# Optimization experiments

Hardware: AMD Instinct MI355X
Metric: run time of the kernel (lower is better)

The kernel has to match this reference:

```python
import jax, jax.numpy as jnp
import numpy as np

B, S, E, H = 4, 4096, 1024, 16
W_SIZE, LB, LF = 128, 1, 1   # window size, look_backward, look_forward (non-causal)
HD = E // H                  # head dim = 64
NW = S // W_SIZE             # num windows = 32
NC = LB + LF + 1             # concatenated windows per query window = 3


def collect_windows(x, backward=LB, forward=LF, pad_value=-1):
    # x: [BH, NW, w] or [BH, NW, w, d]; gather windows i-backward..i+forward
    nw = x.shape[1]
    pad = [(0, 0), (backward, forward)] + [(0, 0)] * (x.ndim - 2)
    xp = jnp.pad(x, pad, constant_values=pad_value)  # faithful: pads k/v with -1 like the torch code
    g = jnp.stack([xp[:, j:j + nw] for j in range(backward + forward + 1)], axis=2)  # [BH,NW,NC,w,...]
    if x.ndim == 4:
        return g.reshape(x.shape[0], nw, NC * x.shape[2], x.shape[3])
    return g.reshape(x.shape[0], nw, NC * x.shape[2])


def setup_inputs() -> dict:
    key = jax.random.key(0)
    k1, k2 = jax.random.split(key)
    x = jax.random.normal(k1, (B, S, E), dtype=jnp.float32)
    w_qkv = jax.random.normal(k2, (E, 3 * E), dtype=jnp.float32) * 0.02
    b_qkv = jnp.zeros((3 * E,), dtype=jnp.float32)
    return {"x": x, "w_qkv": w_qkv, "b_qkv": b_qkv}


def reference(x, w_qkv, b_qkv):
    qkv = x @ w_qkv + b_qkv                                   # [B,S,3E]
    q, k, v = jnp.split(qkv, 3, axis=-1)

    def to_heads(t):
        return t.reshape(B, S, H, HD).transpose(0, 2, 1, 3).reshape(B * H, S, HD)

    q, k, v = to_heads(q), to_heads(k), to_heads(v)

    bq = q.reshape(B * H, NW, W_SIZE, HD)                     # [BH,NW,w,d]
    bk = collect_windows(k.reshape(B * H, NW, W_SIZE, HD))    # [BH,NW,NC*w,d]
    bv = collect_windows(v.reshape(B * H, NW, W_SIZE, HD))

    t = jnp.arange(S, dtype=jnp.int32).reshape(1, NW, W_SIZE)
    ct = collect_windows(t)                                   # [1,NW,NC*w], pads are -1

    # no 1/sqrt(d) scaling in the original module
    scores = jnp.einsum('bnqd,bnkd->bnqk', bq, bk)            # [BH,NW,w,NC*w]

    qi = t.reshape(1, NW, W_SIZE, 1)                          # query absolute positions
    ctb = ct[:, :, None, :]                                   # key absolute positions
    max_i = qi + W_SIZE * LF
    min_i = qi - W_SIZE * LB
    overcompute = ((ctb > max_i) | (ctb < min_i)) & (ctb != -1)

    scores = jnp.where(overcompute, -jnp.inf, scores)
    attn = jax.nn.softmax(scores, axis=-1)
    attn = jnp.nan_to_num(attn, nan=0.0, posinf=0.0, neginf=0.0)

    out = jnp.einsum('bnqk,bnkd->bnqd', attn, bv)             # [BH,NW,w,d]
    out = out.reshape(B, H, S, HD).transpose(0, 2, 1, 3).reshape(B, S, E)
    return out
```

## Files before the change

### kernel.cpp

```cpp
#include <hip/hip_runtime.h>
#include <hip/hip_bf16.h>
#include <cmath>

constexpr int Bn  = 4;
constexpr int Sn  = 4096;
constexpr int En  = 1024;
constexpr int Hn  = 16;
constexpr int HD  = 64;
constexpr int WSZ = 128;
constexpr int NW  = Sn / WSZ;
constexpr int Mr  = Bn * Sn;
constexpr int N3  = 3 * En;
constexpr int Kd  = En;

typedef __attribute__((ext_vector_type(8))) short  bf16x8;
typedef __attribute__((ext_vector_type(4))) float  f32x4;
typedef __attribute__((ext_vector_type(8))) unsigned short ushort8;

__device__ __forceinline__ unsigned short f2bf(float f) {
  __hip_bfloat16 h = __float2bfloat16(f);
  return *reinterpret_cast<unsigned short*>(&h);
}

__device__ __forceinline__ void gload_lds16(const void* g, void* l) {
  __builtin_amdgcn_global_load_lds(
      (const __attribute__((address_space(1))) void*)g,
      (__attribute__((address_space(3))) void*)l, 16, 0, 0);
}

__global__ __launch_bounds__(256) void cvt_x(const float* __restrict__ x,
                                             unsigned short* __restrict__ xb) {
  const int i = (blockIdx.x * 256 + threadIdx.x) * 8;
  const float4 a = *(const float4*)&x[i];
  const float4 b = *(const float4*)&x[i + 4];
  ushort8 o;
  o[0] = f2bf(a.x); o[1] = f2bf(a.y); o[2] = f2bf(a.z); o[3] = f2bf(a.w);
  o[4] = f2bf(b.x); o[5] = f2bf(b.y); o[6] = f2bf(b.z); o[7] = f2bf(b.w);
  *(ushort8*)&xb[i] = o;
}

__global__ __launch_bounds__(256) void cvt_wT(const float* __restrict__ W,
                                              unsigned short* __restrict__ Wt) {
  __shared__ float t[32][33];
  const int bx = blockIdx.x * 32;
  const int by = blockIdx.y * 32;
  const int tx = threadIdx.x & 31;
  const int ty = threadIdx.x >> 5;
  #pragma unroll
  for (int i = 0; i < 32; i += 8)
    t[ty + i][tx] = W[(size_t)(by + ty + i) * N3 + bx + tx];
  __syncthreads();
  #pragma unroll
  for (int i = 0; i < 32; i += 8)
    Wt[(size_t)(bx + ty + i) * Kd + by + tx] = f2bf(t[tx][ty + i]);
}

constexpr int TM = 128, TN = 128, TK = 32;

__global__ __launch_bounds__(256) void qkv_gemm_bf16(
    const unsigned short* __restrict__ Abf,
    const unsigned short* __restrict__ Bt,
    const float* __restrict__ bias,
    unsigned short* __restrict__ Qb, unsigned short* __restrict__ Kb,
    unsigned short* __restrict__ Vb) {
  __shared__ unsigned short As[TM * TK];
  __shared__ unsigned short Bs[TN * TK];

  const int tid  = threadIdx.x;
  const int wave = tid >> 6;
  const int lane = tid & 63;
  const int bm = blockIdx.y * TM;
  const int bn = blockIdx.x * TN;
  const int wr = wave >> 1, wc = wave & 1;

  f32x4 acc[4][4] = {};

  const int sr  = lane >> 2;
  const int sc8 = (lane & 3) * 8;
  const int fr = lane & 15;
  const int fk = (lane >> 4) * 8;

  for (int k0 = 0; k0 < Kd; k0 += TK) {
    #pragma unroll
    for (int i = 0; i < 2; ++i) {
      const int c = wave * 2 + i;
      gload_lds16(Abf + (size_t)(bm + c * 16 + sr) * Kd + k0 + sc8, &As[c * 512]);
      gload_lds16(Bt  + (size_t)(bn + c * 16 + sr) * Kd + k0 + sc8, &Bs[c * 512]);
    }
    __syncthreads();
    bf16x8 af[4], bfr[4];
    #pragma unroll
    for (int m = 0; m < 4; ++m)
      af[m] = *(const bf16x8*)&As[(wr * 64 + m * 16 + fr) * TK + fk];
    #pragma unroll
    for (int n = 0; n < 4; ++n)
      bfr[n] = *(const bf16x8*)&Bs[(wc * 64 + n * 16 + fr) * TK + fk];
    #pragma unroll
    for (int m = 0; m < 4; ++m)
      #pragma unroll
      for (int n = 0; n < 4; ++n)
        acc[m][n] = __builtin_amdgcn_mfma_f32_16x16x32_bf16(
            af[m], bfr[n], acc[m][n], 0, 0, 0);
    __syncthreads();
  }

  const int col0 = bn + wc * 64 + (lane & 15);
  const int row0 = bm + wr * 64 + (lane >> 4) * 4;
  #pragma unroll
  for (int n = 0; n < 4; ++n) {
    const int col = col0 + n * 16;
    const float bv = bias[col];
    const int which = col >> 10;
    const int h = (col >> 6) & 15;
    const int d = col & 63;
    unsigned short* T = (which == 0) ? Qb : (which == 1) ? Kb : Vb;
    #pragma unroll
    for (int m = 0; m < 4; ++m)
      #pragma unroll
      for (int r = 0; r < 4; ++r) {
        const int row = row0 + m * 16 + r;
        const int b = row >> 12;
        const int s = row & 4095;
        T[((size_t)((b << 4) + h) * Sn + s) * HD + d] =
            f2bf(acc[m][n][r] + bv);
      }
  }
}

__global__ __launch_bounds__(256) void attn_mfma(
    const unsigned short* __restrict__ Qb,
    const unsigned short* __restrict__ Kb,
    const unsigned short* __restrict__ Vb,
    float* __restrict__ out) {
  __shared__ unsigned short Qs[128 * 64];
  __shared__ unsigned short Ks[64 * 64];
  __shared__ unsigned short Vt[64 * 64];
  __shared__ unsigned short Ps[4][32 * 72];

  const int w   = blockIdx.x;
  const int bh  = blockIdx.y;
  const int tid = threadIdx.x, wave = tid >> 6, lane = tid & 63;
  const int gl = lane >> 4;
  const int li = lane & 15;
  const int q0 = wave * 32;

  const size_t head_off = (size_t)bh * Sn * HD;
  const unsigned short* Qg = Qb + head_off + (size_t)w * WSZ * HD;

  const int rsub = lane >> 3;
  const int bsub = ((lane & 7) ^ rsub) << 3;
  #pragma unroll
  for (int i = 0; i < 4; ++i) {
    const int c = wave * 4 + i;
    gload_lds16(Qg + (size_t)(c * 8 + rsub) * HD + bsub, &Qs[c * 512]);
  }
  __syncthreads();

  auto lds_frag = [&](const unsigned short* base, int row, int kpos) {
    return *(const bf16x8*)((const char*)base + row * 128 +
                            ((kpos * 2) ^ ((row & 7) << 4)));
  };

  bf16x8 ones;
  #pragma unroll
  for (int j = 0; j < 8; ++j) ones[j] = (short)0x3F80;
  f32x4 qsum[2] = {};
  #pragma unroll
  for (int m = 0; m < 2; ++m)
    #pragma unroll
    for (int ks = 0; ks < 2; ++ks)
      qsum[m] = __builtin_amdgcn_mfma_f32_16x16x32_bf16(
          lds_frag(Qs, q0 + m * 16 + li, ks * 32 + gl * 8), ones, qsum[m], 0, 0, 0);

  f32x4 acc[2][4] = {};
  float m_run[2][4], l_run[2][4];
  #pragma unroll
  for (int m = 0; m < 2; ++m)
    #pragma unroll
    for (int r = 0; r < 4; ++r) { m_run[m][r] = -3e38f; l_run[m][r] = 0.f; }

  unsigned short* Psw = &Ps[wave][0];
  const int vkey = wave * 16 + (lane >> 2);
  const int vd0 = (lane & 3) * 16;

  for (int c = 0; c < 3; ++c) {
    const int wk = w + c - 1;
    if (wk < 0 || wk >= NW) {
      #pragma unroll
      for (int m = 0; m < 2; ++m)
        #pragma unroll
        for (int r = 0; r < 4; ++r) {
          const float sp = -qsum[m][r];
          const float mn = fmaxf(m_run[m][r], sp);
          const float scale = __expf(m_run[m][r] - mn);
          const float pe = __expf(sp - mn) * 128.f;
          l_run[m][r] = l_run[m][r] * scale + pe;
          m_run[m][r] = mn;
          #pragma unroll
          for (int nd = 0; nd < 4; ++nd)
            acc[m][nd][r] = acc[m][nd][r] * scale - pe;
        }
      continue;
    }
    for (int ch = 0; ch < 2; ++ch) {
      __syncthreads();
      const unsigned short* Kg =
          Kb + head_off + (size_t)(wk * WSZ + ch * 64) * HD;
      #pragma unroll
      for (int i = 0; i < 2; ++i) {
        const int cc = wave * 2 + i;
        gload_lds16(Kg + (size_t)(cc * 8 + rsub) * HD + bsub, &Ks[cc * 512]);
      }
      {
        const unsigned short* Vg =
            Vb + head_off + (size_t)(wk * WSZ + ch * 64) * HD;
        const ushort8 v0 = *(const ushort8*)&Vg[vkey * HD + vd0];
        const ushort8 v1 = *(const ushort8*)&Vg[vkey * HD + vd0 + 8];
        #pragma unroll
        for (int j = 0; j < 8; ++j) {
          int d = vd0 + j;
          *(unsigned short*)((char*)Vt + ((d * 128 + vkey * 2) ^ ((d & 7) << 4))) = v0[j];
          d = vd0 + 8 + j;
          *(unsigned short*)((char*)Vt + ((d * 128 + vkey * 2) ^ ((d & 7) << 4))) = v1[j];
        }
      }
      __syncthreads();

      f32x4 s[2][4] = {};
      #pragma unroll
      for (int ks = 0; ks < 2; ++ks) {
        const bf16x8 aq0 = lds_frag(Qs, q0 + li, ks * 32 + gl * 8);
        const bf16x8 aq1 = lds_frag(Qs, q0 + 16 + li, ks * 32 + gl * 8);
        #pragma unroll
        for (int n = 0; n < 4; ++n) {
          const bf16x8 bk = lds_frag(Ks, n * 16 + li, ks * 32 + gl * 8);
          s[0][n] = __builtin_amdgcn_mfma_f32_16x16x32_bf16(aq0, bk, s[0][n], 0, 0, 0);
          s[1][n] = __builtin_amdgcn_mfma_f32_16x16x32_bf16(aq1, bk, s[1][n], 0, 0, 0);
        }
      }
      if (c != 1) {
        #pragma unroll
        for (int m = 0; m < 2; ++m)
          #pragma unroll
          for (int n = 0; n < 4; ++n)
            #pragma unroll
            for (int r = 0; r < 4; ++r) {
              const int q_in = q0 + m * 16 + gl * 4 + r;
              const int k_in = ch * 64 + n * 16 + li;
              const bool bad = (c == 0) ? (k_in < q_in) : (k_in > q_in);
              if (bad) s[m][n][r] = -3e38f;
            }
      }
      #pragma unroll
      for (int m = 0; m < 2; ++m) {
        float mx[4], sc[4], rs[4];
        #pragma unroll
        for (int r = 0; r < 4; ++r)
          mx[r] = fmaxf(fmaxf(s[m][0][r], s[m][1][r]),
                        fmaxf(s[m][2][r], s[m][3][r]));
        #pragma unroll
        for (int off = 1; off < 16; off <<= 1)
          #pragma unroll
          for (int r = 0; r < 4; ++r)
            mx[r] = fmaxf(mx[r], __shfl_xor(mx[r], off));
        #pragma unroll
        for (int r = 0; r < 4; ++r) {
          const float mn = fmaxf(m_run[m][r], mx[r]);
          sc[r] = __expf(m_run[m][r] - mn);
          m_run[m][r] = mn;
          rs[r] = 0.f;
        }
        #pragma unroll
        for (int n = 0; n < 4; ++n)
          #pragma unroll
          for (int r = 0; r < 4; ++r) {
            const float v = s[m][n][r];
            const float p = (v > -1e30f) ? __expf(v - m_run[m][r]) : 0.f;
            s[m][n][r] = p;
            rs[r] += p;
          }
        #pragma unroll
        for (int off = 1; off < 16; off <<= 1)
          #pragma unroll
          for (int r = 0; r < 4; ++r)
            rs[r] += __shfl_xor(rs[r], off);
        #pragma unroll
        for (int r = 0; r < 4; ++r)
          l_run[m][r] = l_run[m][r] * sc[r] + rs[r];
        #pragma unroll
        for (int nd = 0; nd < 4; ++nd)
          #pragma unroll
          for (int r = 0; r < 4; ++r)
            acc[m][nd][r] *= sc[r];
      }
      #pragma unroll
      for (int m = 0; m < 2; ++m)
        #pragma unroll
        for (int n = 0; n < 4; ++n)
          #pragma unroll
          for (int r = 0; r < 4; ++r)
            Psw[(m * 16 + gl * 4 + r) * 72 + n * 16 + li] = f2bf(s[m][n][r]);
      #pragma unroll
      for (int ks = 0; ks < 2; ++ks) {
        const bf16x8 ap0 = *(const bf16x8*)&Psw[(li) * 72 + ks * 32 + gl * 8];
        const bf16x8 ap1 = *(const bf16x8*)&Psw[(16 + li) * 72 + ks * 32 + gl * 8];
        #pragma unroll
        for (int nd = 0; nd < 4; ++nd) {
          const bf16x8 bv = lds_frag(Vt, nd * 16 + li, ks * 32 + gl * 8);
          acc[0][nd] = __builtin_amdgcn_mfma_f32_16x16x32_bf16(ap0, bv, acc[0][nd], 0, 0, 0);
          acc[1][nd] = __builtin_amdgcn_mfma_f32_16x16x32_bf16(ap1, bv, acc[1][nd], 0, 0, 0);
        }
      }
    }
  }

  const int b = bh >> 4, h = bh & 15;
  #pragma unroll
  for (int m = 0; m < 2; ++m) {
    float inv[4];
    #pragma unroll
    for (int r = 0; r < 4; ++r) inv[r] = 1.f / l_run[m][r];
    #pragma unroll
    for (int nd = 0; nd < 4; ++nd)
      #pragma unroll
      for (int r = 0; r < 4; ++r) {
        const int q = q0 + m * 16 + gl * 4 + r;
        out[((size_t)(b * Sn + w * WSZ + q)) * En + h * HD + nd * 16 + li] =
            acc[m][nd][r] * inv[r];
      }
  }
}

extern "C" void kernel_launch(void* const* d_in, const int* in_sizes, int n_in,
                              void* d_out, int out_size, void* d_ws,
                              size_t ws_size, hipStream_t stream) {
  const float* x    = (const float*)d_in[0];
  const float* wqkv = (const float*)d_in[1];
  const float* bqkv = (const float*)d_in[2];
  float* out = (float*)d_out;

  unsigned short* ws = (unsigned short*)d_ws;
  const size_t HT = (size_t)Bn * Hn * Sn * HD;
  unsigned short* Qb = ws;
  unsigned short* Kb = ws + HT;
  unsigned short* Vb = ws + 2 * HT;
  unsigned short* xb = ws + 3 * HT;
  unsigned short* wb = ws + 3 * HT + (size_t)Mr * Kd;

  cvt_x<<<(Mr * Kd) / (256 * 8), 256, 0, stream>>>(x, xb);
  dim3 gw(N3 / 32, Kd / 32);
  cvt_wT<<<gw, 256, 0, stream>>>(wqkv, wb);

  dim3 g1(N3 / TN, Mr / TM);
  qkv_gemm_bf16<<<g1, 256, 0, stream>>>(xb, wb, bqkv, Qb, Kb, Vb);

  dim3 g2(NW, Bn * Hn);
  attn_mfma<<<g2, 256, 0, stream>>>(Qb, Kb, Vb, out);
}
```

Baseline: 415.8 us.

## Double-buffer K/V tiles in attention, pre-transpose V, keep Q in registers

Adds a separate kernel that writes V transposed to [BH, HD, S], so the attention kernel can stage V with async global-to-LDS loads instead of scalar transposing stores. K and V tiles are double-buffered so the next chunk loads while the current one is computed, and the loop needs one barrier per chunk instead of two. Q fragments are loaded straight into registers instead of going through LDS, and MFMA sections get raised wave priority. The cost is an extra kernel launch plus a full extra read and write of V, and more workspace.

```diff
diff --git a/kernel.cpp b/kernel.cpp
--- a/kernel.cpp
+++ b/kernel.cpp
@@ -55,6 +55,26 @@
     Wt[(size_t)(bx + ty + i) * Kd + by + tx] = f2bf(t[tx][ty + i]);
 }
 
+__global__ __launch_bounds__(256) void cvt_vT(const unsigned short* __restrict__ V,
+                                              unsigned short* __restrict__ VT) {
+  __shared__ unsigned short t[64][72];
+  const int s0 = blockIdx.x * 64;
+  const int bh = blockIdx.y;
+  const unsigned short* Vg = V + ((size_t)bh * Sn + s0) * HD;
+  const int r  = threadIdx.x >> 3;
+  const int c8 = (threadIdx.x & 7) * 8;
+  *(ushort8*)&t[r][c8]      = *(const ushort8*)&Vg[(size_t)r * HD + c8];
+  *(ushort8*)&t[r + 32][c8] = *(const ushort8*)&Vg[(size_t)(r + 32) * HD + c8];
+  __syncthreads();
+  unsigned short* Og = VT + (size_t)bh * HD * Sn + s0;
+  const int d = threadIdx.x >> 3;
+  ushort8 o0, o1;
+  #pragma unroll
+  for (int j = 0; j < 8; ++j) { o0[j] = t[c8 + j][d]; o1[j] = t[c8 + j][d + 32]; }
+  *(ushort8*)&Og[(size_t)d * Sn + c8]        = o0;
+  *(ushort8*)&Og[(size_t)(d + 32) * Sn + c8] = o1;
+}
+
 constexpr int TM = 128, TN = 128, TK = 32;
 
 __global__ __launch_bounds__(256) void qkv_gemm_bf16(
@@ -130,188 +150,201 @@
 __global__ __launch_bounds__(256) void attn_mfma(
     const unsigned short* __restrict__ Qb,
     const unsigned short* __restrict__ Kb,
-    const unsigned short* __restrict__ Vb,
+    const unsigned short* __restrict__ VT,
     float* __restrict__ out) {
-  __shared__ unsigned short Qs[128 * 64];
-  __shared__ unsigned short Ks[64 * 64];
-  __shared__ unsigned short Vt[64 * 64];
+  __shared__ unsigned short Ks[2][64 * 64];
+  __shared__ unsigned short Vs[2][64 * 64];
   __shared__ unsigned short Ps[4][32 * 72];
 
   const int w   = blockIdx.x;
   const int bh  = blockIdx.y;
   const int tid = threadIdx.x, wave = tid >> 6, lane = tid & 63;
-  const int gl = lane >> 4;
-  const int li = lane & 15;
+  const int gl = lane >> 4, li = lane & 15;
   const int q0 = wave * 32;
 
   const size_t head_off = (size_t)bh * Sn * HD;
-  const unsigned short* Qg = Qb + head_off + (size_t)w * WSZ * HD;
-
-  const int rsub = lane >> 3;
-  const int bsub = ((lane & 7) ^ rsub) << 3;
-  #pragma unroll
-  for (int i = 0; i < 4; ++i) {
-    const int c = wave * 4 + i;
-    gload_lds16(Qg + (size_t)(c * 8 + rsub) * HD + bsub, &Qs[c * 512]);
-  }
-  __syncthreads();
+  const unsigned short* Qg  = Qb + head_off + (size_t)w * WSZ * HD;
+  const unsigned short* Kg0 = Kb + head_off;
+  const unsigned short* Vg0 = VT + (size_t)bh * HD * Sn;
+
+  bf16x8 qf[2][2];
+  #pragma unroll
+  for (int m = 0; m < 2; ++m)
+    #pragma unroll
+    for (int ks = 0; ks < 2; ++ks)
+      qf[m][ks] = *(const bf16x8*)
+          &Qg[(size_t)(q0 + m * 16 + li) * HD + ks * 32 + gl * 8];
+
+  bf16x8 ones;
+  #pragma unroll
+  for (int j = 0; j < 8; ++j) ones[j] = (short)0x3F80;
+  f32x4 qsum[2] = {};
+  #pragma unroll
+  for (int m = 0; m < 2; ++m)
+    #pragma unroll
+    for (int ks = 0; ks < 2; ++ks)
+      qsum[m] = __builtin_amdgcn_mfma_f32_16x16x32_bf16(
+          qf[m][ks], ones, qsum[m], 0, 0, 0);
+
+  f32x4 acc[2][4] = {};
+  float m_run[2][4], l_run[2][4];
+  #pragma unroll
+  for (int m = 0; m < 2; ++m)
+    #pragma unroll
+    for (int r = 0; r < 4; ++r) { m_run[m][r] = -3e38f; l_run[m][r] = 0.f; }
+
+  if (w == 0 || w == NW - 1) {
+    #pragma unroll
+    for (int m = 0; m < 2; ++m)
+      #pragma unroll
+      for (int r = 0; r < 4; ++r) {
+        const float sp = -qsum[m][r];
+        const float mn = fmaxf(m_run[m][r], sp);
+        const float scale = __expf(m_run[m][r] - mn);
+        const float pe = __expf(sp - mn) * 128.f;
+        l_run[m][r] = l_run[m][r] * scale + pe;
+        m_run[m][r] = mn;
+        #pragma unroll
+        for (int nd = 0; nd < 4; ++nd)
+          acc[m][nd][r] = acc[m][nd][r] * scale - pe;
+      }
+  }
+
+  int vw[3], nv = 0;
+  #pragma unroll
+  for (int c = 0; c < 3; ++c) {
+    const int wk = w + c - 1;
+    if (0 <= wk && wk < NW) vw[nv++] = wk;
+  }
+  const int T = 2 * nv;
+
+  const int rsub  = lane >> 3;
+  const int ebsub = ((lane & 7) ^ rsub) * 8;
+
+  auto stage = [&](int t, int buf) {
+    const int wk = vw[t >> 1];
+    const int s0 = wk * WSZ + (t & 1) * 64;
+    #pragma unroll
+    for (int i = 0; i < 2; ++i) {
+      const int cc = wave * 2 + i;
+      gload_lds16(Kg0 + (size_t)(s0 + cc * 8 + rsub) * HD + ebsub,
+                  &Ks[buf][cc * 512]);
+      gload_lds16(Vg0 + (size_t)(cc * 8 + rsub) * Sn + s0 + ebsub,
+                  &Vs[buf][cc * 512]);
+    }
+  };
 
   auto lds_frag = [&](const unsigned short* base, int row, int kpos) {
     return *(const bf16x8*)((const char*)base + row * 128 +
                             ((kpos * 2) ^ ((row & 7) << 4)));
   };
 
-  bf16x8 ones;
-  #pragma unroll
-  for (int j = 0; j < 8; ++j) ones[j] = (short)0x3F80;
-  f32x4 qsum[2] = {};
-  #pragma unroll
-  for (int m = 0; m < 2; ++m)
-    #pragma unroll
-    for (int ks = 0; ks < 2; ++ks)
-      qsum[m] = __builtin_amdgcn_mfma_f32_16x16x32_bf16(
-          lds_frag(Qs, q0 + m * 16 + li, ks * 32 + gl * 8), ones, qsum[m], 0, 0, 0);
-
-  f32x4 acc[2][4] = {};
-  float m_run[2][4], l_run[2][4];
-  #pragma unroll
-  for (int m = 0; m < 2; ++m)
-    #pragma unroll
-    for (int r = 0; r < 4; ++r) { m_run[m][r] = -3e38f; l_run[m][r] = 0.f; }
-
   unsigned short* Psw = &Ps[wave][0];
-  const int vkey = wave * 16 + (lane >> 2);
-  const int vd0 = (lane & 3) * 16;
-
-  for (int c = 0; c < 3; ++c) {
-    const int wk = w + c - 1;
-    if (wk < 0 || wk >= NW) {
+
+  stage(0, 0);
+  __syncthreads();
+
+  for (int t = 0; t < T; ++t) {
+    const int buf = t & 1;
+    if (t + 1 < T) stage(t + 1, buf ^ 1);
+
+    const int wk = vw[t >> 1];
+    const int c  = wk - w + 1;
+    const int ch = t & 1;
+
+    f32x4 s[2][4] = {};
+    __builtin_amdgcn_s_setprio(1);
+    #pragma unroll
+    for (int ks = 0; ks < 2; ++ks) {
+      #pragma unroll
+      for (int n = 0; n < 4; ++n) {
+        const bf16x8 bk = lds_frag(&Ks[buf][0], n * 16 + li, ks * 32 + gl * 8);
+        s[0][n] = __builtin_amdgcn_mfma_f32_16x16x32_bf16(qf[0][ks], bk, s[0][n], 0, 0, 0);
+        s[1][n] = __builtin_amdgcn_mfma_f32_16x16x32_bf16(qf[1][ks], bk, s[1][n], 0, 0, 0);
+      }
+    }
+    __builtin_amdgcn_s_setprio(0);
+
+    if (c != 1) {
       #pragma unroll
       for (int m = 0; m < 2; ++m)
-        #pragma unroll
-        for (int r = 0; r < 4; ++r) {
-          const float sp = -qsum[m][r];
-          const float mn = fmaxf(m_run[m][r], sp);
-          const float scale = __expf(m_run[m][r] - mn);
-          const float pe = __expf(sp - mn) * 128.f;
-          l_run[m][r] = l_run[m][r] * scale + pe;
-          m_run[m][r] = mn;
-          #pragma unroll
-          for (int nd = 0; nd < 4; ++nd)
-            acc[m][nd][r] = acc[m][nd][r] * scale - pe;
-        }
-      continue;
-    }
-    for (int ch = 0; ch < 2; ++ch) {
-      __syncthreads();
-      const unsigned short* Kg =
-          Kb + head_off + (size_t)(wk * WSZ + ch * 64) * HD;
-      #pragma unroll
-      for (int i = 0; i < 2; ++i) {
-        const int cc = wave * 2 + i;
-        gload_lds16(Kg + (size_t)(cc * 8 + rsub) * HD + bsub, &Ks[cc * 512]);
-      }
-      {
-        const unsigned short* Vg =
-            Vb + head_off + (size_t)(wk * WSZ + ch * 64) * HD;
-        const ushort8 v0 = *(const ushort8*)&Vg[vkey * HD + vd0];
-        const ushort8 v1 = *(const ushort8*)&Vg[vkey * HD + vd0 + 8];
-        #pragma unroll
-        for (int j = 0; j < 8; ++j) {
-          int d = vd0 + j;
-          *(unsigned short*)((char*)Vt + ((d * 128 + vkey * 2) ^ ((d & 7) << 4))) = v0[j];
-          d = vd0 + 8 + j;
-          *(unsigned short*)((char*)Vt + ((d * 128 + vkey * 2) ^ ((d & 7) << 4))) = v1[j];
-        }
-      }
-      __syncthreads();
-
-      f32x4 s[2][4] = {};
-      #pragma unroll
-      for (int ks = 0; ks < 2; ++ks) {
-        const bf16x8 aq0 = lds_frag(Qs, q0 + li, ks * 32 + gl * 8);
-        const bf16x8 aq1 = lds_frag(Qs, q0 + 16 + li, ks * 32 + gl * 8);
-        #pragma unroll
-        for (int n = 0; n < 4; ++n) {
-          const bf16x8 bk = lds_frag(Ks, n * 16 + li, ks * 32 + gl * 8);
-          s[0][n] = __builtin_amdgcn_mfma_f32_16x16x32_bf16(aq0, bk, s[0][n], 0, 0, 0);
-          s[1][n] = __builtin_amdgcn_mfma_f32_16x16x32_bf16(aq1, bk, s[1][n], 0, 0, 0);
-        }
-      }
-      if (c != 1) {
-        #pragma unroll
-        for (int m = 0; m < 2; ++m)
-          #pragma unroll
-          for (int n = 0; n < 4; ++n)
-            #pragma unroll
-            for (int r = 0; r < 4; ++r) {
-              const int q_in = q0 + m * 16 + gl * 4 + r;
-              const int k_in = ch * 64 + n * 16 + li;
-              const bool bad = (c == 0) ? (k_in < q_in) : (k_in > q_in);
-              if (bad) s[m][n][r] = -3e38f;
-            }
-      }
-      #pragma unroll
-      for (int m = 0; m < 2; ++m) {
-        float mx[4], sc[4], rs[4];
-        #pragma unroll
-        for (int r = 0; r < 4; ++r)
-          mx[r] = fmaxf(fmaxf(s[m][0][r], s[m][1][r]),
-                        fmaxf(s[m][2][r], s[m][3][r]));
-        #pragma unroll
-        for (int off = 1; off < 16; off <<= 1)
-          #pragma unroll
-          for (int r = 0; r < 4; ++r)
-            mx[r] = fmaxf(mx[r], __shfl_xor(mx[r], off));
-        #pragma unroll
-        for (int r = 0; r < 4; ++r) {
-          const float mn = fmaxf(m_run[m][r], mx[r]);
-          sc[r] = __expf(m_run[m][r] - mn);
-          m_run[m][r] = mn;
-          rs[r] = 0.f;
-        }
         #pragma unroll
         for (int n = 0; n < 4; ++n)
           #pragma unroll
           for (int r = 0; r < 4; ++r) {
-            const float v = s[m][n][r];
-            const float p = (v > -1e30f) ? __expf(v - m_run[m][r]) : 0.f;
-            s[m][n][r] = p;
-            rs[r] += p;
+            const int q_in = q0 + m * 16 + gl * 4 + r;
+            const int k_in = ch * 64 + n * 16 + li;
+            const bool bad = (c == 0) ? (k_in < q_in) : (k_in > q_in);
+            if (bad) s[m][n][r] = -3e38f;
           }
-        #pragma unroll
-        for (int off = 1; off < 16; off <<= 1)
-          #pragma unroll
-          for (int r = 0; r < 4; ++r)
-            rs[r] += __shfl_xor(rs[r], off);
+    }
+
+    #pragma unroll
+    for (int m = 0; m < 2; ++m) {
+      float mx[4], sc[4], rs[4];
+      #pragma unroll
+      for (int r = 0; r < 4; ++r)
+        mx[r] = fmaxf(fmaxf(s[m][0][r], s[m][1][r]),
+                      fmaxf(s[m][2][r], s[m][3][r]));
+      #pragma unroll
+      for (int off = 1; off < 16; off <<= 1)
         #pragma unroll
         for (int r = 0; r < 4; ++r)
-          l_run[m][r] = l_run[m][r] * sc[r] + rs[r];
-        #pragma unroll
-        for (int nd = 0; nd < 4; ++nd)
-          #pragma unroll
-          for (int r = 0; r < 4; ++r)
-            acc[m][nd][r] *= sc[r];
-      }
-      #pragma unroll
-      for (int m = 0; m < 2; ++m)
-        #pragma unroll
-        for (int n = 0; n < 4; ++n)
-          #pragma unroll
-          for (int r = 0; r < 4; ++r)
-            Psw[(m * 16 + gl * 4 + r) * 72 + n * 16 + li] = f2bf(s[m][n][r]);
-      #pragma unroll
-      for (int ks = 0; ks < 2; ++ks) {
-        const bf16x8 ap0 = *(const bf16x8*)&Psw[(li) * 72 + ks * 32 + gl * 8];
-        const bf16x8 ap1 = *(const bf16x8*)&Psw[(16 + li) * 72 + ks * 32 + gl * 8];
-        #pragma unroll
-        for (int nd = 0; nd < 4; ++nd) {
-          const bf16x8 bv = lds_frag(Vt, nd * 16 + li, ks * 32 + gl * 8);
-          acc[0][nd] = __builtin_amdgcn_mfma_f32_16x16x32_bf16(ap0, bv, acc[0][nd], 0, 0, 0);
-          acc[1][nd] = __builtin_amdgcn_mfma_f32_16x16x32_bf16(ap1, bv, acc[1][nd], 0, 0, 0);
+          mx[r] = fmaxf(mx[r], __shfl_xor(mx[r], off));
+      #pragma unroll
+      for (int r = 0; r < 4; ++r) {
+        const float mn = fmaxf(m_run[m][r], mx[r]);
+        sc[r] = __expf(m_run[m][r] - mn);
+        m_run[m][r] = mn;
+        rs[r] = 0.f;
+      }
+      #pragma unroll
+      for (int n = 0; n < 4; ++n)
+        #pragma unroll
+        for (int r = 0; r < 4; ++r) {
+          const float v = s[m][n][r];
+          const float p = (v > -1e30f) ? __expf(v - m_run[m][r]) : 0.f;
+          s[m][n][r] = p;
+          rs[r] += p;
         }
-      }
-    }
+      #pragma unroll
+      for (int off = 1; off < 16; off <<= 1)
+        #pragma unroll
+        for (int r = 0; r < 4; ++r)
+          rs[r] += __shfl_xor(rs[r], off);
+      #pragma unroll
+      for (int r = 0; r < 4; ++r)
+        l_run[m][r] = l_run[m][r] * sc[r] + rs[r];
+      #pragma unroll
+      for (int nd = 0; nd < 4; ++nd)
+        #pragma unroll
+        for (int r = 0; r < 4; ++r)
+          acc[m][nd][r] *= sc[r];
+    }
+
+    #pragma unroll
+    for (int m = 0; m < 2; ++m)
+      #pragma unroll
+      for (int n = 0; n < 4; ++n)
+        #pragma unroll
+        for (int r = 0; r < 4; ++r)
+          Psw[(m * 16 + gl * 4 + r) * 72 + n * 16 + li] = f2bf(s[m][n][r]);
+
+    __builtin_amdgcn_s_setprio(1);
+    #pragma unroll
+    for (int ks = 0; ks < 2; ++ks) {
+      const bf16x8 ap0 = *(const bf16x8*)&Psw[(li) * 72 + ks * 32 + gl * 8];
+      const bf16x8 ap1 = *(const bf16x8*)&Psw[(16 + li) * 72 + ks * 32 + gl * 8];
+      #pragma unroll
+      for (int nd = 0; nd < 4; ++nd) {
+        const bf16x8 bv = lds_frag(&Vs[buf][0], nd * 16 + li, ks * 32 + gl * 8);
+        acc[0][nd] = __builtin_amdgcn_mfma_f32_16x16x32_bf16(ap0, bv, acc[0][nd], 0, 0, 0);
+        acc[1][nd] = __builtin_amdgcn_mfma_f32_16x16x32_bf16(ap1, bv, acc[1][nd], 0, 0, 0);
+      }
+    }
+    __builtin_amdgcn_s_setprio(0);
+
+    __syncthreads();
   }
 
   const int b = bh >> 4, h = bh & 15;
@@ -344,8 +377,9 @@
   unsigned short* Qb = ws;
   unsigned short* Kb = ws + HT;
   unsigned short* Vb = ws + 2 * HT;
-  unsigned short* xb = ws + 3 * HT;
-  unsigned short* wb = ws + 3 * HT + (size_t)Mr * Kd;
+  unsigned short* VTt = ws + 3 * HT;
+  unsigned short* xb = ws + 4 * HT;
+  unsigned short* wb = ws + 4 * HT + (size_t)Mr * Kd;
 
   cvt_x<<<(Mr * Kd) / (256 * 8), 256, 0, stream>>>(x, xb);
   dim3 gw(N3 / 32, Kd / 32);
@@ -354,6 +388,9 @@
   dim3 g1(N3 / TN, Mr / TM);
   qkv_gemm_bf16<<<g1, 256, 0, stream>>>(xb, wb, bqkv, Qb, Kb, Vb);
 
+  dim3 gv(Sn / 64, Bn * Hn);
+  cvt_vT<<<gv, 256, 0, stream>>>(Vb, VTt);
+
   dim3 g2(NW, Bn * Hn);
-  attn_mfma<<<g2, 256, 0, stream>>>(Qb, Kb, Vb, out);
-}
+  attn_mfma<<<g2, 256, 0, stream>>>(Qb, Kb, VTt, out);
+}
```

Result: faster. 386.8 us (-7.0%).
